# Optimization experiments

Hardware: AMD Instinct MI355X
Metric: run time of the kernel (lower is better)

## Reference

```python
import jax, jax.numpy as jnp
import numpy as np

N = 262144       # batch rows
C = 256          # in_channels
K = 256          # uint8 code range


def setup_inputs() -> dict:
    key = jax.random.key(0)
    k1, k2, k3, k4 = jax.random.split(key, 4)
    left = jax.random.randint(k1, (N, C), 0, K, dtype=jnp.int32)
    right = jax.random.randint(k2, (N, C), 0, K, dtype=jnp.int32)
    # per-channel 256x256 lookup tables: white_table[c][l, r] -> new code in [0, 256)
    white_table = jax.random.randint(k3, (C, K, K), 0, K, dtype=jnp.int32)
    # per-channel last-layer codebook: last_codebook[c][1][code] -> float
    codebook = jax.random.normal(k4, (C, K), dtype=jnp.float32)
    return {"left": left, "right": right, "white_table": white_table, "codebook": codebook}


def reference(left, right, white_table, codebook):
    # Fused equivalent of the per-channel python loop:
    #   for c: codes[:, c] = white_table[c][left[:, c], right[:, c]]
    #   out[:, c]  = codebook[c][codes[:, c]]
    ch = jnp.arange(C, dtype=jnp.int32)[None, :]          # [1, C] broadcasts vs [N, C]
    codes = white_table[ch, left, right]                   # [N, C] int32 gather
    out = codebook[ch, codes]                              # [N, C] float32 gather
    return out
```

## Files before the change

kernel.cpp:

```cpp
#include <hip/hip_runtime.h>
#include <stdint.h>

#define CCH 256
#define KK  256

typedef int   i32x4 __attribute__((ext_vector_type(4)));
typedef float f32x4 __attribute__((ext_vector_type(4)));
typedef unsigned short u16x8 __attribute__((ext_vector_type(8)));

__global__ __launch_bounds__(256) void compress_table_kernel(
    const int4* __restrict__ t, uchar4* __restrict__ o, int n4) {
  int i = blockIdx.x * 256 + threadIdx.x;
  if (i < n4) {
    int4 v = t[i];
    o[i] = make_uchar4((unsigned char)v.x, (unsigned char)v.y,
                       (unsigned char)v.z, (unsigned char)v.w);
  }
}

__global__ __launch_bounds__(256) void transpose_pack_kernel(
    const int* __restrict__ L, const int* __restrict__ R,
    unsigned short* __restrict__ LRt, int n0_base, int nslice) {
  __shared__ unsigned short tile[64][66];
  const int ntn  = nslice >> 6;
  const int tn   = blockIdx.x % ntn;
  const int tc   = blockIdx.x / ntn;
  const int lane = threadIdx.x & 63;
  const int ty   = threadIdx.x >> 6;
  const int gn0  = n0_base + tn * 64;
  const int c0   = tc * 64;
#pragma unroll
  for (int p = 0; p < 16; ++p) {
    const int n = p * 4 + ty;
    const size_t gi = (size_t)(gn0 + n) * CCH + c0 + lane;
    tile[lane][n] = (unsigned short)((L[gi] << 8) | R[gi]);
  }
  __syncthreads();
#pragma unroll
  for (int p = 0; p < 16; ++p) {
    const int ch = p * 4 + ty;
    LRt[(size_t)(c0 + ch) * nslice + tn * 64 + lane] = tile[ch][lane];
  }
}

__global__ __launch_bounds__(256) void code_gather_kernel(
    const unsigned short* __restrict__ LRt, const unsigned char* __restrict__ tab8,
    unsigned char* __restrict__ codes, int nslice, int nsub) {
  __shared__ unsigned char tabs[KK * KK];
  const int c   = blockIdx.x & (CCH - 1);
  const int sub = blockIdx.x >> 8;
  const int chunk = nslice / nsub;
  {
    const int4* src = (const int4*)(tab8 + (size_t)c * (KK * KK));
    int4* dst = (int4*)tabs;
#pragma unroll
    for (int i = 0; i < 16; ++i) dst[threadIdx.x + 256 * i] = src[threadIdx.x + 256 * i];
  }
  __syncthreads();
  const size_t base = (size_t)c * nslice + (size_t)sub * chunk;
  const u16x8* __restrict__ in   = (const u16x8*)(LRt + base);
  uint2*       __restrict__ outp = (uint2*)(codes + base);
  const int iters = chunk >> 13;
  for (int it = 0; it < iters; ++it) {
    u16x8 v0 = in[(it * 4 + 0) * 256 + threadIdx.x];
    u16x8 v1 = in[(it * 4 + 1) * 256 + threadIdx.x];
    u16x8 v2 = in[(it * 4 + 2) * 256 + threadIdx.x];
    u16x8 v3 = in[(it * 4 + 3) * 256 + threadIdx.x];
#define PACK8(v, slot)                                                         \
    {                                                                          \
      unsigned lo = (unsigned)tabs[v[0]] | ((unsigned)tabs[v[1]] << 8) |       \
                    ((unsigned)tabs[v[2]] << 16) | ((unsigned)tabs[v[3]] << 24);\
      unsigned hi = (unsigned)tabs[v[4]] | ((unsigned)tabs[v[5]] << 8) |       \
                    ((unsigned)tabs[v[6]] << 16) | ((unsigned)tabs[v[7]] << 24);\
      outp[(it * 4 + slot) * 256 + threadIdx.x] = make_uint2(lo, hi);          \
    }
    PACK8(v0, 0) PACK8(v1, 1) PACK8(v2, 2) PACK8(v3, 3)
#undef PACK8
  }
}

__global__ __launch_bounds__(256) void codebook_transpose_kernel(
    const unsigned char* __restrict__ codes, const float* __restrict__ cb,
    float* __restrict__ out, int n0_base, int nslice) {
  __shared__ float cbs[32 * KK];
  __shared__ unsigned int ctile[32 * 65];
  const int ntiles = nslice >> 8;
  const int tn = blockIdx.x % ntiles;
  const int tc = blockIdx.x / ntiles;
  const int c0 = tc * 32;
  {
    const f32x4* cbg = (const f32x4*)(cb + (size_t)c0 * KK);
    f32x4* cbl = (f32x4*)cbs;
#pragma unroll
    for (int i = 0; i < 8; ++i) cbl[threadIdx.x + 256 * i] = cbg[threadIdx.x + 256 * i];
  }
  {
    const int lane = threadIdx.x & 63;
    const int ty   = threadIdx.x >> 6;
    const size_t nbase = (size_t)tn * 256;
#pragma unroll
    for (int p = 0; p < 8; ++p) {
      const int cc = p * 4 + ty;
      const unsigned v =
          ((const unsigned*)(codes + (size_t)(c0 + cc) * nslice + nbase))[lane];
      ctile[cc * 65 + lane] = v;
    }
  }
  __syncthreads();
  const unsigned char* ct8 = (const unsigned char*)ctile;
  const int cc  = threadIdx.x & 31;
  const int nn0 = threadIdx.x >> 5;
  const float* cbrow = cbs + cc * KK;
  float* orow = out + (size_t)(n0_base + tn * 256) * CCH + c0 + cc;
#pragma unroll 4
  for (int p = 0; p < 32; ++p) {
    const int n = p * 8 + nn0;
    const unsigned code = ct8[cc * 260 + n];
    orow[(size_t)n * CCH] = cbrow[code];
  }
}

#define ROWS_PER_BLOCK 512
#define NGROUPS 16
#define GCH (CCH / NGROUPS)

template <typename TabT>
__global__ __launch_bounds__(256, 8) void gather_kernel(
    const i32x4* __restrict__ left, const i32x4* __restrict__ right,
    const TabT* __restrict__ tab, const float* __restrict__ cb,
    f32x4* __restrict__ out, int nrows) {
  __shared__ float cbs[GCH * KK];
  const int g     = blockIdx.x & (NGROUPS - 1);
  const int chunk = blockIdx.x / NGROUPS;
  const int q     = threadIdx.x & 3;
  const int rsub  = threadIdx.x >> 2;
  {
    const f32x4* cbg = (const f32x4*)(cb + (size_t)(g * GCH) * KK);
    f32x4* cbl = (f32x4*)cbs;
#pragma unroll
    for (int i = 0; i < 4; ++i) cbl[threadIdx.x + i * 256] = cbg[threadIdx.x + i * 256];
  }
  __syncthreads();
  const int cbase  = g * GCH + q * 4;
  const TabT* t0   = tab + (size_t)cbase * (KK * KK);
  const int vecoff = g * 4 + q;
  const float* cq  = cbs + (q * 4) * KK;
  const int rbase = chunk * ROWS_PER_BLOCK;
#pragma unroll
  for (int it = 0; it < ROWS_PER_BLOCK / 32; ++it) {
    const int r0 = rbase + it * 32 + rsub;
    if (r0 >= nrows) break;
    const unsigned v0 = (unsigned)r0 * 64u + (unsigned)vecoff;
    i32x4 L0 = left[v0];
    i32x4 R0 = right[v0];
    unsigned c0 = (unsigned)t0[          (unsigned)(L0[0] * KK + R0[0])];
    unsigned c1 = (unsigned)t0[ 65536u + (unsigned)(L0[1] * KK + R0[1])];
    unsigned c2 = (unsigned)t0[131072u + (unsigned)(L0[2] * KK + R0[2])];
    unsigned c3 = (unsigned)t0[196608u + (unsigned)(L0[3] * KK + R0[3])];
    f32x4 o;
    o[0] = cq[       c0];
    o[1] = cq[KK   + c1];
    o[2] = cq[2*KK + c2];
    o[3] = cq[3*KK + c3];
    ((f32x4*)out)[v0] = o;
  }
}

extern "C" void kernel_launch(void* const* d_in, const int* in_sizes, int n_in,
                              void* d_out, int out_size, void* d_ws, size_t ws_size,
                              hipStream_t stream) {
  const int*   left  = (const int*)d_in[0];
  const int*   right = (const int*)d_in[1];
  const int*   wt    = (const int*)d_in[2];
  const float* cb    = (const float*)d_in[3];
  float* out = (float*)d_out;

  const int nrows = in_sizes[0] / CCH;
  const int tab_elems = CCH * KK * KK;
  const size_t tab_bytes = (size_t)tab_elems;

  int S = 0;
  for (int s = 1; s <= 32; s <<= 1) {
    if (nrows % (s * 8192)) continue;
    size_t need = tab_bytes + (size_t)768 * (size_t)(nrows / s);
    if (need <= ws_size) { S = s; break; }
  }

  if (S) {
    unsigned char* tab8 = (unsigned char*)d_ws;
    int n4 = tab_elems / 4;
    compress_table_kernel<<<n4 / 256, 256, 0, stream>>>(
        (const int4*)wt, (uchar4*)tab8, n4);

    const int nslice = nrows / S;
    unsigned short* LRt = (unsigned short*)((char*)d_ws + tab_bytes);
    unsigned char* codes = (unsigned char*)d_ws + tab_bytes + (size_t)512 * nslice;
    const int nsub = (nslice >= 32768) ? (nslice / 32768) : 1;

    for (int h = 0; h < S; ++h) {
      const int n0 = h * nslice;
      transpose_pack_kernel<<<(nslice / 64) * 4, 256, 0, stream>>>(
          left, right, LRt, n0, nslice);
      code_gather_kernel<<<nsub * CCH, 256, 0, stream>>>(
          LRt, tab8, codes, nslice, nsub);
      codebook_transpose_kernel<<<(nslice / 256) * 8, 256, 0, stream>>>(
          codes, cb, out, n0, nslice);
    }
  } else if (ws_size >= tab_bytes) {
    unsigned char* tab8 = (unsigned char*)d_ws;
    int n4 = tab_elems / 4;
    compress_table_kernel<<<n4 / 256, 256, 0, stream>>>(
        (const int4*)wt, (uchar4*)tab8, n4);
    const int blocks = ((nrows + ROWS_PER_BLOCK - 1) / ROWS_PER_BLOCK) * NGROUPS;
    gather_kernel<unsigned char><<<blocks, 256, 0, stream>>>(
        (const i32x4*)left, (const i32x4*)right, tab8, cb, (f32x4*)out, nrows);
  } else {
    const int blocks = ((nrows + ROWS_PER_BLOCK - 1) / ROWS_PER_BLOCK) * NGROUPS;
    gather_kernel<int><<<blocks, 256, 0, stream>>>(
        (const i32x4*)left, (const i32x4*)right, wt, cb, (f32x4*)out, nrows);
  }
}
```

Baseline: 740.5 us.

## Retile transpose, code-gather and codebook kernels with vector loads and nontemporal stores

The transpose-pack kernel now has each block handle 64 rows across all 256 channels. It uses 16-byte vector loads of left/right, an XOR-swizzled LDS tile and 16-byte vector stores, where before it did scalar loads per 64x64 tile. The code-gather kernel uses 512-thread blocks that each process a fixed 16384-element chunk with no loop, which raises block count and parallelism. The codebook kernel handles 16 channels per block, unpacks four codes per word and writes output with nontemporal stores. Slice sizing now requires multiples of 16384 rows, so the table reloads per block and the occupancy balance change.

Measured after the change: 756.9 us. 1.02x slower.

```diff
diff --git a/kernel.cpp b/kernel.cpp
--- a/kernel.cpp
+++ b/kernel.cpp
@@ -6,6 +6,7 @@
 
 typedef int   i32x4 __attribute__((ext_vector_type(4)));
 typedef float f32x4 __attribute__((ext_vector_type(4)));
+typedef unsigned short u16x4 __attribute__((ext_vector_type(4)));
 typedef unsigned short u16x8 __attribute__((ext_vector_type(8)));
 
 __global__ __launch_bounds__(256) void compress_table_kernel(
@@ -18,105 +19,112 @@
   }
 }
 
-__global__ __launch_bounds__(256) void transpose_pack_kernel(
-    const int* __restrict__ L, const int* __restrict__ R,
+__global__ __launch_bounds__(256, 4) void transpose_pack_kernel(
+    const i32x4* __restrict__ L4, const i32x4* __restrict__ R4,
     unsigned short* __restrict__ LRt, int n0_base, int nslice) {
-  __shared__ unsigned short tile[64][66];
-  const int ntn  = nslice >> 6;
-  const int tn   = blockIdx.x % ntn;
-  const int tc   = blockIdx.x / ntn;
+  __shared__ unsigned short tile[64 * 260];
+  const int tn   = blockIdx.x;
+  const int gn0  = n0_base + tn * 64;
   const int lane = threadIdx.x & 63;
-  const int ty   = threadIdx.x >> 6;
-  const int gn0  = n0_base + tn * 64;
-  const int c0   = tc * 64;
+  const int wid  = threadIdx.x >> 6;
+
 #pragma unroll
   for (int p = 0; p < 16; ++p) {
-    const int n = p * 4 + ty;
-    const size_t gi = (size_t)(gn0 + n) * CCH + c0 + lane;
-    tile[lane][n] = (unsigned short)((L[gi] << 8) | R[gi]);
-  }
-  __syncthreads();
-#pragma unroll
-  for (int p = 0; p < 16; ++p) {
-    const int ch = p * 4 + ty;
-    LRt[(size_t)(c0 + ch) * nslice + tn * 64 + lane] = tile[ch][lane];
-  }
-}
-
-__global__ __launch_bounds__(256) void code_gather_kernel(
+    const int r = p * 4 + wid;
+    const size_t gi = (size_t)(gn0 + r) * 64 + lane;
+    i32x4 Lv = L4[gi];
+    i32x4 Rv = R4[gi];
+    u16x4 w;
+    w[0] = (unsigned short)((Lv[0] << 8) | Rv[0]);
+    w[1] = (unsigned short)((Lv[1] << 8) | Rv[1]);
+    w[2] = (unsigned short)((Lv[2] << 8) | Rv[2]);
+    w[3] = (unsigned short)((Lv[3] << 8) | Rv[3]);
+    const int col = (lane * 4) ^ (((r >> 3) & 7) << 2);
+    *(u16x4*)&tile[r * 260 + col] = w;
+  }
+  __syncthreads();
+
+#pragma unroll
+  for (int pb = 0; pb < 8; ++pb) {
+    const int ch = pb * 32 + (threadIdx.x >> 3);
+    const int n8 = threadIdx.x & 7;
+    u16x8 v;
+#pragma unroll
+    for (int j = 0; j < 8; ++j) {
+      const int r = n8 * 8 + j;
+      v[j] = tile[r * 260 + (ch ^ (n8 << 2))];
+    }
+    *(u16x8*)&LRt[(size_t)ch * nslice + tn * 64 + n8 * 8] = v;
+  }
+}
+
+__global__ __launch_bounds__(512, 4) void code_gather_kernel(
     const unsigned short* __restrict__ LRt, const unsigned char* __restrict__ tab8,
-    unsigned char* __restrict__ codes, int nslice, int nsub) {
+    unsigned char* __restrict__ codes, int nslice) {
   __shared__ unsigned char tabs[KK * KK];
   const int c   = blockIdx.x & (CCH - 1);
   const int sub = blockIdx.x >> 8;
-  const int chunk = nslice / nsub;
   {
     const int4* src = (const int4*)(tab8 + (size_t)c * (KK * KK));
     int4* dst = (int4*)tabs;
 #pragma unroll
-    for (int i = 0; i < 16; ++i) dst[threadIdx.x + 256 * i] = src[threadIdx.x + 256 * i];
-  }
-  __syncthreads();
-  const size_t base = (size_t)c * nslice + (size_t)sub * chunk;
+    for (int i = 0; i < 8; ++i) dst[threadIdx.x + 512 * i] = src[threadIdx.x + 512 * i];
+  }
+  __syncthreads();
+  const size_t base = (size_t)c * nslice + (size_t)sub * 16384;
   const u16x8* __restrict__ in   = (const u16x8*)(LRt + base);
   uint2*       __restrict__ outp = (uint2*)(codes + base);
-  const int iters = chunk >> 13;
-  for (int it = 0; it < iters; ++it) {
-    u16x8 v0 = in[(it * 4 + 0) * 256 + threadIdx.x];
-    u16x8 v1 = in[(it * 4 + 1) * 256 + threadIdx.x];
-    u16x8 v2 = in[(it * 4 + 2) * 256 + threadIdx.x];
-    u16x8 v3 = in[(it * 4 + 3) * 256 + threadIdx.x];
-#define PACK8(v, slot)                                                         \
-    {                                                                          \
-      unsigned lo = (unsigned)tabs[v[0]] | ((unsigned)tabs[v[1]] << 8) |       \
-                    ((unsigned)tabs[v[2]] << 16) | ((unsigned)tabs[v[3]] << 24);\
-      unsigned hi = (unsigned)tabs[v[4]] | ((unsigned)tabs[v[5]] << 8) |       \
-                    ((unsigned)tabs[v[6]] << 16) | ((unsigned)tabs[v[7]] << 24);\
-      outp[(it * 4 + slot) * 256 + threadIdx.x] = make_uint2(lo, hi);          \
-    }
-    PACK8(v0, 0) PACK8(v1, 1) PACK8(v2, 2) PACK8(v3, 3)
+  u16x8 v0 = in[          threadIdx.x];
+  u16x8 v1 = in[ 512 +    threadIdx.x];
+  u16x8 v2 = in[1024 +    threadIdx.x];
+  u16x8 v3 = in[1536 +    threadIdx.x];
+#define PACK8(v, slot)                                                          \
+  {                                                                             \
+    unsigned lo = (unsigned)tabs[v[0]] | ((unsigned)tabs[v[1]] << 8) |          \
+                  ((unsigned)tabs[v[2]] << 16) | ((unsigned)tabs[v[3]] << 24);  \
+    unsigned hi = (unsigned)tabs[v[4]] | ((unsigned)tabs[v[5]] << 8) |          \
+                  ((unsigned)tabs[v[6]] << 16) | ((unsigned)tabs[v[7]] << 24);  \
+    outp[slot * 512 + threadIdx.x] = make_uint2(lo, hi);                        \
+  }
+  PACK8(v0, 0) PACK8(v1, 1) PACK8(v2, 2) PACK8(v3, 3)
 #undef PACK8
-  }
 }
 
 __global__ __launch_bounds__(256) void codebook_transpose_kernel(
     const unsigned char* __restrict__ codes, const float* __restrict__ cb,
     float* __restrict__ out, int n0_base, int nslice) {
-  __shared__ float cbs[32 * KK];
-  __shared__ unsigned int ctile[32 * 65];
+  __shared__ float cbs[16 * KK];
+  __shared__ unsigned ctd[16 * 66];
   const int ntiles = nslice >> 8;
   const int tn = blockIdx.x % ntiles;
   const int tc = blockIdx.x / ntiles;
-  const int c0 = tc * 32;
+  const int c0 = tc * 16;
   {
     const f32x4* cbg = (const f32x4*)(cb + (size_t)c0 * KK);
     f32x4* cbl = (f32x4*)cbs;
 #pragma unroll
-    for (int i = 0; i < 8; ++i) cbl[threadIdx.x + 256 * i] = cbg[threadIdx.x + 256 * i];
-  }
-  {
-    const int lane = threadIdx.x & 63;
-    const int ty   = threadIdx.x >> 6;
-    const size_t nbase = (size_t)tn * 256;
-#pragma unroll
-    for (int p = 0; p < 8; ++p) {
-      const int cc = p * 4 + ty;
-      const unsigned v =
-          ((const unsigned*)(codes + (size_t)(c0 + cc) * nslice + nbase))[lane];
-      ctile[cc * 65 + lane] = v;
+    for (int i = 0; i < 4; ++i) cbl[threadIdx.x + 256 * i] = cbg[threadIdx.x + 256 * i];
+  }
+  {
+    const int cc = threadIdx.x >> 4, l16 = threadIdx.x & 15;
+    const unsigned* row =
+        (const unsigned*)(codes + (size_t)(c0 + cc) * nslice + (size_t)tn * 256);
+#pragma unroll
+    for (int q = 0; q < 4; ++q) ctd[cc * 66 + q * 16 + l16] = row[q * 16 + l16];
+  }
+  __syncthreads();
+  const int cc = threadIdx.x & 15, nn4 = threadIdx.x >> 4;
+  const float* cbrow = cbs + cc * KK;
+  float* obase = out + (size_t)(n0_base + tn * 256) * CCH + c0 + cc;
+#pragma unroll
+  for (int p = 0; p < 4; ++p) {
+    const int d = p * 16 + nn4;
+    const unsigned c4v = ctd[cc * 66 + d];
+#pragma unroll
+    for (int k = 0; k < 4; ++k) {
+      const float val = cbrow[(c4v >> (8 * k)) & 255u];
+      __builtin_nontemporal_store(val, obase + (size_t)(d * 4 + k) * CCH);
     }
-  }
-  __syncthreads();
-  const unsigned char* ct8 = (const unsigned char*)ctile;
-  const int cc  = threadIdx.x & 31;
-  const int nn0 = threadIdx.x >> 5;
-  const float* cbrow = cbs + cc * KK;
-  float* orow = out + (size_t)(n0_base + tn * 256) * CCH + c0 + cc;
-#pragma unroll 4
-  for (int p = 0; p < 32; ++p) {
-    const int n = p * 8 + nn0;
-    const unsigned code = ct8[cc * 260 + n];
-    orow[(size_t)n * CCH] = cbrow[code];
   }
 }
 
@@ -162,7 +170,7 @@
     o[1] = cq[KK   + c1];
     o[2] = cq[2*KK + c2];
     o[3] = cq[3*KK + c3];
-    ((f32x4*)out)[v0] = o;
+    out[v0] = o;
   }
 }
 
@@ -180,8 +188,8 @@
   const size_t tab_bytes = (size_t)tab_elems;
 
   int S = 0;
-  for (int s = 1; s <= 32; s <<= 1) {
-    if (nrows % (s * 8192)) continue;
+  for (int s = 1; s <= 16; s <<= 1) {
+    if (nrows % (s * 16384)) continue;
     size_t need = tab_bytes + (size_t)768 * (size_t)(nrows / s);
     if (need <= ws_size) { S = s; break; }
   }
@@ -195,15 +203,14 @@
     const int nslice = nrows / S;
     unsigned short* LRt = (unsigned short*)((char*)d_ws + tab_bytes);
     unsigned char* codes = (unsigned char*)d_ws + tab_bytes + (size_t)512 * nslice;
-    const int nsub = (nslice >= 32768) ? (nslice / 32768) : 1;
 
     for (int h = 0; h < S; ++h) {
       const int n0 = h * nslice;
-      transpose_pack_kernel<<<(nslice / 64) * 4, 256, 0, stream>>>(
-          left, right, LRt, n0, nslice);
-      code_gather_kernel<<<nsub * CCH, 256, 0, stream>>>(
-          LRt, tab8, codes, nslice, nsub);
-      codebook_transpose_kernel<<<(nslice / 256) * 8, 256, 0, stream>>>(
+      transpose_pack_kernel<<<nslice / 64, 256, 0, stream>>>(
+          (const i32x4*)left, (const i32x4*)right, LRt, n0, nslice);
+      code_gather_kernel<<<(nslice / 16384) * CCH, 512, 0, stream>>>(
+          LRt, tab8, codes, nslice);
+      codebook_transpose_kernel<<<(nslice / 256) * 16, 256, 0, stream>>>(
           codes, cb, out, n0, nslice);
     }
   } else if (ws_size >= tab_bytes) {
```
